# Optimization experiments

Hardware: AMD Instinct MI355X
Metric: run time of the kernel (lower is better)

Reference implementation:

```python
import jax, jax.numpy as jnp
import numpy as np

B, S, D_IN, H, SD = 512, 1024, 64, 64, 4


def setup_inputs() -> dict:
    key = jax.random.key(0)
    ks = jax.random.split(key, 12)
    sc_in = 1.0 / np.sqrt(D_IN)
    sc_h = 1.0 / np.sqrt(H)
    sc_c = 1.0 / np.sqrt(SD + H)
    return {
        "x": jax.random.normal(ks[0], (B, S, D_IN), jnp.float32),
        "W1": jax.random.uniform(ks[1], (H, D_IN), jnp.float32, -sc_in, sc_in),
        "b1": jax.random.uniform(ks[2], (H,), jnp.float32, -sc_in, sc_in),
        "ln_g": jnp.ones((H,), jnp.float32),
        "ln_b": jnp.zeros((H,), jnp.float32),
        "Wi": jax.random.uniform(ks[3], (SD, H), jnp.float32, -sc_h, sc_h),
        "bi": jax.random.uniform(ks[4], (SD,), jnp.float32, -sc_h, sc_h),
        "Wc1": jax.random.uniform(ks[5], (H, SD + H), jnp.float32, -sc_c, sc_c),
        "bc1": jax.random.uniform(ks[6], (H,), jnp.float32, -sc_c, sc_c),
        "Wc2": jax.random.uniform(ks[7], (SD, H), jnp.float32, -sc_h, sc_h),
        "bc2": jax.random.uniform(ks[8], (SD,), jnp.float32, -sc_h, sc_h),
        "corr_scale": jnp.asarray(0.01, jnp.float32),
        "A_level": jnp.zeros((1,), jnp.float32),
        "A_trend": jnp.zeros((1,), jnp.float32),
        "A_gamma": jnp.zeros((1,), jnp.float32),
        "A_resid": jnp.zeros((1,), jnp.float32),
        "omega": jnp.zeros((1,), jnp.float32),
    }


def reference(x, W1, b1, ln_g, ln_b, Wi, bi, Wc1, bc1, Wc2, bc2,
              corr_scale, A_level, A_trend, A_gamma, A_resid, omega):
    # input_proj: Linear -> LayerNorm -> GELU (exact erf), dropout=0
    h = jnp.einsum('bsd,hd->bsh', x, W1) + b1
    mu = jnp.mean(h, axis=-1, keepdims=True)
    var = jnp.mean((h - mu) ** 2, axis=-1, keepdims=True)
    h = (h - mu) * jax.lax.rsqrt(var + 1e-5) * ln_g + ln_b
    h = jax.nn.gelu(h, approximate=False)  # [B,S,H]

    # structured A for state_dim == 4: diag(a_l, a_t, gamma*cos(w), a_r)
    a_l = jax.nn.sigmoid(A_level) * 0.15 + 0.85
    a_t = jax.nn.sigmoid(A_trend) * 0.25 + 0.7
    gamma = jax.nn.sigmoid(A_gamma) * 0.2 + 0.8
    a_r = jax.nn.sigmoid(A_resid) * 0.4
    A = jnp.diag(jnp.concatenate([a_l, a_t, gamma * jnp.cos(omega), a_r]))  # [4,4]

    # innovation applied to all steps at once (batched tiny GEMM)
    bx = jnp.einsum('bsh,kh->bsk', h, Wi) + bi  # [B,S,4]

    def step(s, inp):
        bx_t, h_t = inp  # [B,4], [B,H]
        s_lin = s @ A.T + bx_t
        corr_in = jnp.concatenate([s_lin, h_t], axis=-1)  # [B,4+H]
        c = jax.nn.gelu(corr_in @ Wc1.T + bc1, approximate=False) @ Wc2.T + bc2
        s_new = s_lin + corr_scale * jnp.tanh(c)
        return s_new, s_new

    s0 = jnp.zeros((x.shape[0], SD), x.dtype)
    _, outs = jax.lax.scan(step, s0, (bx.transpose(1, 0, 2), h.transpose(1, 0, 2)))
    return outs.transpose(1, 0, 2)  # [B,S,4] == return_all_states=True
```

## Files before the change

### kernel.cpp

```cpp
#include <hip/hip_runtime.h>
#include <hip/hip_bf16.h>

#define BB 512
#define SS 1024
#define DIN 64
#define HH 64
#define SD4 4
#define CH 64
#define LB 64

typedef __attribute__((ext_vector_type(8))) short s8v;
typedef __attribute__((ext_vector_type(4))) float f4v;

#define MFMA_BF16(a, b, c) __builtin_amdgcn_mfma_f32_16x16x32_bf16((a), (b), (c), 0, 0, 0)

template <int CTRL>
__device__ __forceinline__ float dppf(float v) {
    return __int_as_float(__builtin_amdgcn_mov_dpp(__float_as_int(v), CTRL, 0xF, 0xF, false));
}

__device__ __forceinline__ float rcp_fast(float x) {
    return __builtin_amdgcn_rcpf(x);
}
__device__ __forceinline__ unsigned int cvt_pk(float lo, float hi) {
    unsigned int r;
    asm("v_cvt_pk_bf16_f32 %0, %1, %2" : "=v"(r) : "v"(lo), "v"(hi));
    return r;
}
__device__ __forceinline__ float bf2f(unsigned short u) {
    return __uint_as_float(((unsigned int)u) << 16);
}
__device__ __forceinline__ float sigmoid_f(float x) {
    return 1.0f / (1.0f + __expf(-x));
}
__device__ __forceinline__ float tanh_fast(float x) {
    return fmaf(-2.0f, rcp_fast(__expf(2.0f * x) + 1.0f), 1.0f);
}
__device__ __forceinline__ float gelu_fast(float x) {
    float x2 = x * x;
    float z = x * fmaf(x2, -0.0713548162f, -1.5957691216f);
    return x * rcp_fast(1.0f + __expf(z));
}
__device__ __forceinline__ s8v cvt8(const float* __restrict__ p) {
    const float4* q4 = (const float4*)p;
    float4 a = q4[0], b = q4[1];
    union { s8v s; unsigned int u[4]; } r;
    r.u[0] = cvt_pk(a.x, a.y); r.u[1] = cvt_pk(a.z, a.w);
    r.u[2] = cvt_pk(b.x, b.y); r.u[3] = cvt_pk(b.z, b.w);
    return r.s;
}

__global__ __launch_bounds__(256)
void prep_mfma(const float* __restrict__ x,
               const float* __restrict__ W1, const float* __restrict__ b1,
               const float* __restrict__ ln_g, const float* __restrict__ ln_b,
               const float* __restrict__ Wi, const float* __restrict__ bi,
               const float* __restrict__ Wc1, const float* __restrict__ bc1,
               uint2* __restrict__ pre4, float* __restrict__ bx)
{
    __shared__ unsigned short hb[4][16 * 88];
    __shared__ unsigned short wcs[64 * 72];

    const int tid = threadIdx.x;
    const int wave = tid >> 6;
    const int lane = tid & 63;
    const int c = lane & 15;
    const int q = lane >> 4;

    const long tokW = ((long)blockIdx.x * 4 + wave) * 64;

    const float* xp = x + (tokW + c) * DIN + q * 8;
    float4 xf0 = *(const float4*)(xp + 0);
    float4 xf1 = *(const float4*)(xp + 4);
    float4 xf2 = *(const float4*)(xp + 32);
    float4 xf3 = *(const float4*)(xp + 36);
    xp += 16 * DIN;

    {
        const int row = tid >> 2, chn = tid & 3;
        const float4* s4 = (const float4*)(Wc1 + row * 68 + 4 + chn * 16);
        float4 f0 = s4[0], f1 = s4[1], f2 = s4[2], f3 = s4[3];
        uint2* dst = (uint2*)(wcs + row * 72 + chn * 16);
        dst[0] = make_uint2(cvt_pk(f0.x, f0.y), cvt_pk(f0.z, f0.w));
        dst[1] = make_uint2(cvt_pk(f1.x, f1.y), cvt_pk(f1.z, f1.w));
        dst[2] = make_uint2(cvt_pk(f2.x, f2.y), cvt_pk(f2.z, f2.w));
        dst[3] = make_uint2(cvt_pk(f3.x, f3.y), cvt_pk(f3.z, f3.w));
    }
    __syncthreads();

    s8v W1f[4][2], Wif[2];
#pragma unroll
    for (int n = 0; n < 4; ++n)
#pragma unroll
        for (int kh = 0; kh < 2; ++kh)
            W1f[n][kh] = cvt8(W1 + (4 * c + n) * DIN + q * 8 + kh * 32);
#pragma unroll
    for (int kh = 0; kh < 2; ++kh) {
        if (c < 4) {
            Wif[kh] = cvt8(Wi + c * HH + q * 8 + kh * 32);
        } else {
            s8v z;
#pragma unroll
            for (int e = 0; e < 8; ++e) z[e] = 0;
            Wif[kh] = z;
        }
    }

    float gln[4], bln[4], b1v[4], bc1v[4];
#pragma unroll
    for (int n = 0; n < 4; ++n) {
        const int j1 = 4 * c + n;
        const int j2 = c + 16 * n;
        gln[n] = ln_g[j1]; bln[n] = ln_b[j1]; b1v[n] = b1[j1];
        bc1v[n] = bc1[j2];
    }
    const float biv = (c < 4) ? bi[c] : 0.0f;

    unsigned short* Hb = hb[wave];
    uint2* pq = pre4 + (tokW + q * 4) * 16 + c;
    float* bq = bx + (tokW + q * 4) * SD4 + c;

    auto gemm1_ln = [&](s8v A0_, s8v A1_, uint2* hwo) {
        f4v acc[4];
#pragma unroll
        for (int n = 0; n < 4; ++n) {
            f4v z = { b1v[n], b1v[n], b1v[n], b1v[n] };
            z = MFMA_BF16(A0_, W1f[n][0], z);
            acc[n] = MFMA_BF16(A1_, W1f[n][1], z);
        }
        float sm[4], sq[4];
#pragma unroll
        for (int r = 0; r < 4; ++r) {
            sm[r] = acc[0][r] + acc[1][r] + acc[2][r] + acc[3][r];
            sq[r] = fmaf(acc[0][r], acc[0][r],
                    fmaf(acc[1][r], acc[1][r],
                    fmaf(acc[2][r], acc[2][r], acc[3][r] * acc[3][r])));
        }
#pragma unroll
        for (int r = 0; r < 4; ++r) { sm[r] += dppf<0x121>(sm[r]); sq[r] += dppf<0x121>(sq[r]); }
#pragma unroll
        for (int r = 0; r < 4; ++r) { sm[r] += dppf<0x122>(sm[r]); sq[r] += dppf<0x122>(sq[r]); }
#pragma unroll
        for (int r = 0; r < 4; ++r) { sm[r] += dppf<0x124>(sm[r]); sq[r] += dppf<0x124>(sq[r]); }
#pragma unroll
        for (int r = 0; r < 4; ++r) { sm[r] += dppf<0x128>(sm[r]); sq[r] += dppf<0x128>(sq[r]); }
#pragma unroll
        for (int r = 0; r < 4; ++r) {
            const float mu = sm[r] * (1.0f / HH);
            const float var = fmaf(-mu, mu, sq[r] * (1.0f / HH));
            const float rstd = rsqrtf(var + 1e-5f);
            float g0 = gelu_fast(fmaf((acc[0][r] - mu) * rstd, gln[0], bln[0]));
            float g1 = gelu_fast(fmaf((acc[1][r] - mu) * rstd, gln[1], bln[1]));
            float g2 = gelu_fast(fmaf((acc[2][r] - mu) * rstd, gln[2], bln[2]));
            float g3 = gelu_fast(fmaf((acc[3][r] - mu) * rstd, gln[3], bln[3]));
            hwo[r] = make_uint2(cvt_pk(g0, g1), cvt_pk(g2, g3));
        }
    };

    s8v A0, A1;
    {
        union { s8v s; unsigned int u[4]; } a;
        a.u[0] = cvt_pk(xf0.x, xf0.y); a.u[1] = cvt_pk(xf0.z, xf0.w);
        a.u[2] = cvt_pk(xf1.x, xf1.y); a.u[3] = cvt_pk(xf1.z, xf1.w);
        A0 = a.s;
        a.u[0] = cvt_pk(xf2.x, xf2.y); a.u[1] = cvt_pk(xf2.z, xf2.w);
        a.u[2] = cvt_pk(xf3.x, xf3.y); a.u[3] = cvt_pk(xf3.z, xf3.w);
        A1 = a.s;
    }
    xf0 = *(const float4*)(xp + 0);
    xf1 = *(const float4*)(xp + 4);
    xf2 = *(const float4*)(xp + 32);
    xf3 = *(const float4*)(xp + 36);
    xp += 16 * DIN;

    uint2 hw[4];
    gemm1_ln(A0, A1, hw);
#pragma unroll
    for (int r = 0; r < 4; ++r) *(uint2*)(Hb + (q * 4 + r) * 88 + 4 * c) = hw[r];

#pragma unroll 1
    for (int t = 0; t < 4; ++t) {
        s8v H0 = *(const s8v*)(Hb + c * 88 + q * 8);
        s8v H1 = *(const s8v*)(Hb + c * 88 + 32 + q * 8);

        uint2 hwn[4];
        if (t < 3) {
            union { s8v s; unsigned int u[4]; } a;
            a.u[0] = cvt_pk(xf0.x, xf0.y); a.u[1] = cvt_pk(xf0.z, xf0.w);
            a.u[2] = cvt_pk(xf1.x, xf1.y); a.u[3] = cvt_pk(xf1.z, xf1.w);
            s8v nA0 = a.s;
            a.u[0] = cvt_pk(xf2.x, xf2.y); a.u[1] = cvt_pk(xf2.z, xf2.w);
            a.u[2] = cvt_pk(xf3.x, xf3.y); a.u[3] = cvt_pk(xf3.z, xf3.w);
            s8v nA1 = a.s;
            if (t < 2) {
                xf0 = *(const float4*)(xp + 0);
                xf1 = *(const float4*)(xp + 4);
                xf2 = *(const float4*)(xp + 32);
                xf3 = *(const float4*)(xp + 36);
                xp += 16 * DIN;
            }
            gemm1_ln(nA0, nA1, hwn);
        }

        f4v p[4];
#pragma unroll
        for (int n = 0; n < 4; ++n) {
            const s8v Wf0 = *(const s8v*)(wcs + (c + 16 * n) * 72 + q * 8);
            const s8v Wf1 = *(const s8v*)(wcs + (c + 16 * n) * 72 + 32 + q * 8);
            f4v z = { bc1v[n], bc1v[n], bc1v[n], bc1v[n] };
            z = MFMA_BF16(H0, Wf0, z);
            p[n] = MFMA_BF16(H1, Wf1, z);
        }
        f4v bz = { biv, biv, biv, biv };
        bz = MFMA_BF16(H0, Wif[0], bz);
        bz = MFMA_BF16(H1, Wif[1], bz);

        if (c < 4) {
#pragma unroll
            for (int r = 0; r < 4; ++r) bq[r * SD4] = bz[r];
        }
#pragma unroll
        for (int r = 0; r < 4; ++r)
            pq[r * 16] = make_uint2(cvt_pk(p[0][r], p[1][r]),
                                    cvt_pk(p[2][r], p[3][r]));
        pq += 256; bq += 64;

        if (t < 3) {
#pragma unroll
            for (int r = 0; r < 4; ++r) *(uint2*)(Hb + (q * 4 + r) * 88 + 4 * c) = hwn[r];
        }
    }
}

__global__ __launch_bounds__(256)
void scan_chunk(const uint2* __restrict__ pre4, const float* __restrict__ bx,
                const float* __restrict__ Wc1, const float* __restrict__ Wc2,
                const float* __restrict__ bc2, const float* __restrict__ corr_scale,
                const float* __restrict__ A_level, const float* __restrict__ A_trend,
                const float* __restrict__ A_gamma, const float* __restrict__ A_resid,
                const float* __restrict__ omega, float* __restrict__ out)
{
    const int tid = threadIdx.x;
    const int task = blockIdx.x * 16 + (tid >> 4);
    const int L = tid & 15;
    const int ci = task >> 9;
    const int b = task & 511;
    const int warm = (ci * CH < LB) ? ci * CH : LB;
    const int t0 = ci * CH - warm;
    const int nsteps = warm + CH;

    float w[4][4], v[4][4];
#pragma unroll
    for (int m = 0; m < 4; ++m) {
        const int j = L + 16 * m;
#pragma unroll
        for (int k = 0; k < 4; ++k) {
            w[m][k] = Wc1[j * 68 + k];
            v[k][m] = Wc2[k * HH + j];
        }
    }
    const float cs = corr_scale[0];
    const float a0 = sigmoid_f(A_level[0]) * 0.15f + 0.85f;
    const float a1 = sigmoid_f(A_trend[0]) * 0.25f + 0.70f;
    const float a2 = (sigmoid_f(A_gamma[0]) * 0.2f + 0.8f) * cosf(omega[0]);
    const float a3 = sigmoid_f(A_resid[0]) * 0.4f;
    const float csel = bc2[L & 3];
    const bool o1 = (L & 1) != 0;
    const bool o2 = (L & 2) != 0;

    const uint2* pp = pre4 + ((long)b * SS + t0) * 16 + L;
    const float4* bp = (const float4*)bx + (long)b * SS + t0;
    float* op = out + ((long)b * SS + t0) * SD4;

    float s0 = 0.f, s1 = 0.f, s2 = 0.f, s3 = 0.f;

    uint2 pv[4]; float4 bv[4];
#pragma unroll
    for (int i = 0; i < 4; ++i) { pv[i] = pp[(long)i * 16]; bv[i] = bp[i]; }

#pragma unroll 2
    for (int tt = 0; tt < nsteps; tt += 4) {
        const int ntt = (tt + 4 < nsteps) ? (tt + 4) : (nsteps - 4);
        const uint2* qp = pp + (long)ntt * 16;
        const float4* qb = bp + ntt;
        uint2 np[4]; float4 nb[4];
#pragma unroll
        for (int i = 0; i < 4; ++i) { np[i] = qp[i * 16]; nb[i] = qb[i]; }

        const bool wr = (tt >= warm);
#pragma unroll
        for (int i = 0; i < 4; ++i) {
            const float l0 = fmaf(a0, s0, bv[i].x);
            const float l1 = fmaf(a1, s1, bv[i].y);
            const float l2 = fmaf(a2, s2, bv[i].z);
            const float l3 = fmaf(a3, s3, bv[i].w);
            const float p0 = bf2f((unsigned short)(pv[i].x & 0xffffu));
            const float p1 = bf2f((unsigned short)(pv[i].x >> 16));
            const float p2 = bf2f((unsigned short)(pv[i].y & 0xffffu));
            const float p3 = bf2f((unsigned short)(pv[i].y >> 16));
            float g[4];
            {
                float ua0 = fmaf(l0, w[0][0], p0), ub0 = fmaf(l2, w[0][2], l3 * w[0][3]);
                float ua1 = fmaf(l0, w[1][0], p1), ub1 = fmaf(l2, w[1][2], l3 * w[1][3]);
                float ua2 = fmaf(l0, w[2][0], p2), ub2 = fmaf(l2, w[2][2], l3 * w[2][3]);
                float ua3 = fmaf(l0, w[3][0], p3), ub3 = fmaf(l2, w[3][2], l3 * w[3][3]);
                g[0] = gelu_fast(fmaf(l1, w[0][1], ua0) + ub0);
                g[1] = gelu_fast(fmaf(l1, w[1][1], ua1) + ub1);
                g[2] = gelu_fast(fmaf(l1, w[2][1], ua2) + ub2);
                g[3] = gelu_fast(fmaf(l1, w[3][1], ua3) + ub3);
            }
            const float P0 = fmaf(g[0], v[0][0], g[1] * v[0][1]) + fmaf(g[2], v[0][2], g[3] * v[0][3]);
            const float P1 = fmaf(g[0], v[1][0], g[1] * v[1][1]) + fmaf(g[2], v[1][2], g[3] * v[1][3]);
            const float P2 = fmaf(g[0], v[2][0], g[1] * v[2][1]) + fmaf(g[2], v[2][2], g[3] * v[2][3]);
            const float P3 = fmaf(g[0], v[3][0], g[1] * v[3][1]) + fmaf(g[2], v[3][2], g[3] * v[3][3]);
            const float k0 = o1 ? P1 : P0, s0s = o1 ? P0 : P1;
            const float k1 = o1 ? P3 : P2, s1s = o1 ? P2 : P3;
            const float Af = k0 + dppf<0xB1>(s0s);
            const float Bf = k1 + dppf<0xB1>(s1s);
            const float kk = o2 ? Bf : Af, ss = o2 ? Af : Bf;
            float T = kk + dppf<0x4E>(ss);
            T += dppf<0x124>(T);
            T += dppf<0x128>(T);
            const float th = tanh_fast(T + csel);
            const float lsel = o2 ? (o1 ? l3 : l2) : (o1 ? l1 : l0);
            const float sval = fmaf(cs, th, lsel);
            s0 = dppf<0x00>(sval);
            s1 = dppf<0x55>(sval);
            s2 = dppf<0xAA>(sval);
            s3 = dppf<0xFF>(sval);
            if (wr && L < 4) op[(tt + i) * SD4 + L] = sval;
        }
#pragma unroll
        for (int i = 0; i < 4; ++i) { pv[i] = np[i]; bv[i] = nb[i]; }
    }
}

extern "C" void kernel_launch(void* const* d_in, const int* in_sizes, int n_in,
                              void* d_out, int out_size, void* d_ws, size_t ws_size,
                              hipStream_t stream) {
    (void)in_sizes; (void)n_in; (void)out_size; (void)ws_size;
    const float* x    = (const float*)d_in[0];
    const float* W1   = (const float*)d_in[1];
    const float* b1   = (const float*)d_in[2];
    const float* ln_g = (const float*)d_in[3];
    const float* ln_b = (const float*)d_in[4];
    const float* Wi   = (const float*)d_in[5];
    const float* bi   = (const float*)d_in[6];
    const float* Wc1  = (const float*)d_in[7];
    const float* bc1  = (const float*)d_in[8];
    const float* Wc2  = (const float*)d_in[9];
    const float* bc2  = (const float*)d_in[10];
    const float* corr = (const float*)d_in[11];
    const float* Al   = (const float*)d_in[12];
    const float* At   = (const float*)d_in[13];
    const float* Ag   = (const float*)d_in[14];
    const float* Ar   = (const float*)d_in[15];
    const float* om   = (const float*)d_in[16];

    uint2* pre4 = (uint2*)d_ws;
    float* bx = (float*)((char*)d_ws + (size_t)BB * SS * 16 * sizeof(uint2));
    float* out = (float*)d_out;

    prep_mfma<<<dim3(2048), dim3(256), 0, stream>>>(
        x, W1, b1, ln_g, ln_b, Wi, bi, Wc1, bc1, pre4, bx);
    scan_chunk<<<dim3(BB * SS / CH / 16), dim3(256), 0, stream>>>(
        pre4, bx, Wc1, Wc2, bc2, corr, Al, At, Ag, Ar, om, out);
}
```

Measured before the change: 298.2 us.

## Reorder pre-activation layout for 16-byte loads and map one batch row per block

The prep kernel now writes the bf16 pre-activations in a token-quad-major layout with two 16-byte stores per lane instead of four 8-byte stores. The scan reads each 4-step group with wide uint4 loads and launches one block per batch row, with each 16-lane group handling one chunk. Each group runs a fixed 128-step loop (64 warm-up plus 64 output steps). Outputs are gathered into one register per lane and written as a single coalesced store per 4 steps. The trade-offs are fewer blocks, redundant steps for chunk 0 (now 128 instead of 64), and a two-deep prefetch with unroll 1.

```diff
diff --git a/kernel.cpp b/kernel.cpp
--- a/kernel.cpp
+++ b/kernel.cpp
@@ -117,7 +117,7 @@
     const float biv = (c < 4) ? bi[c] : 0.0f;
 
     unsigned short* Hb = hb[wave];
-    uint2* pq = pre4 + (tokW + q * 4) * 16 + c;
+    uint2* pq = pre4 + ((tokW >> 2) + q) * 64 + c * 4;
     float* bq = bx + (tokW + q * 4) * SD4 + c;
 
     auto gemm1_ln = [&](s8v A0_, s8v A1_, uint2* hwo) {
@@ -219,10 +219,14 @@
 #pragma unroll
             for (int r = 0; r < 4; ++r) bq[r * SD4] = bz[r];
         }
-#pragma unroll
-        for (int r = 0; r < 4; ++r)
-            pq[r * 16] = make_uint2(cvt_pk(p[0][r], p[1][r]),
-                                    cvt_pk(p[2][r], p[3][r]));
+        {
+            uint2 u0 = make_uint2(cvt_pk(p[0][0], p[1][0]), cvt_pk(p[2][0], p[3][0]));
+            uint2 u1 = make_uint2(cvt_pk(p[0][1], p[1][1]), cvt_pk(p[2][1], p[3][1]));
+            uint2 u2 = make_uint2(cvt_pk(p[0][2], p[1][2]), cvt_pk(p[2][2], p[3][2]));
+            uint2 u3 = make_uint2(cvt_pk(p[0][3], p[1][3]), cvt_pk(p[2][3], p[3][3]));
+            *(uint4*)(pq)     = make_uint4(u0.x, u0.y, u1.x, u1.y);
+            *(uint4*)(pq + 2) = make_uint4(u2.x, u2.y, u3.x, u3.y);
+        }
         pq += 256; bq += 64;
 
         if (t < 3) {
@@ -241,13 +245,13 @@
                 const float* __restrict__ omega, float* __restrict__ out)
 {
     const int tid = threadIdx.x;
-    const int task = blockIdx.x * 16 + (tid >> 4);
+    const int g = tid >> 4;
     const int L = tid & 15;
-    const int ci = task >> 9;
-    const int b = task & 511;
-    const int warm = (ci * CH < LB) ? ci * CH : LB;
-    const int t0 = ci * CH - warm;
-    const int nsteps = warm + CH;
+    const int b = blockIdx.x;
+    const int warm = (g == 0) ? 0 : LB;
+    const int t0 = g * CH - warm;
+    const int wend = warm + CH;
+    const int myi = L >> 2;
 
     float w[4][4], v[4][4];
 #pragma unroll
@@ -268,51 +272,41 @@
     const bool o1 = (L & 1) != 0;
     const bool o2 = (L & 2) != 0;
 
-    const uint2* pp = pre4 + ((long)b * SS + t0) * 16 + L;
+    const uint4* pp = (const uint4*)pre4 + (((long)b * SS + t0) >> 2) * 32 + L * 2;
     const float4* bp = (const float4*)bx + (long)b * SS + t0;
     float* op = out + ((long)b * SS + t0) * SD4;
 
     float s0 = 0.f, s1 = 0.f, s2 = 0.f, s3 = 0.f;
 
-    uint2 pv[4]; float4 bv[4];
-#pragma unroll
-    for (int i = 0; i < 4; ++i) { pv[i] = pp[(long)i * 16]; bv[i] = bp[i]; }
-
-#pragma unroll 2
-    for (int tt = 0; tt < nsteps; tt += 4) {
-        const int ntt = (tt + 4 < nsteps) ? (tt + 4) : (nsteps - 4);
-        const uint2* qp = pp + (long)ntt * 16;
-        const float4* qb = bp + ntt;
-        uint2 np[4]; float4 nb[4];
-#pragma unroll
-        for (int i = 0; i < 4; ++i) { np[i] = qp[i * 16]; nb[i] = qb[i]; }
-
-        const bool wr = (tt >= warm);
+    auto step4 = [&](uint4 qa, uint4 qb, const float4* bv, int tt) {
+        float oreg = 0.f;
 #pragma unroll
         for (int i = 0; i < 4; ++i) {
+            const unsigned int ux = (i == 0) ? qa.x : (i == 1) ? qa.z : (i == 2) ? qb.x : qb.z;
+            const unsigned int uy = (i == 0) ? qa.y : (i == 1) ? qa.w : (i == 2) ? qb.y : qb.w;
             const float l0 = fmaf(a0, s0, bv[i].x);
             const float l1 = fmaf(a1, s1, bv[i].y);
             const float l2 = fmaf(a2, s2, bv[i].z);
             const float l3 = fmaf(a3, s3, bv[i].w);
-            const float p0 = bf2f((unsigned short)(pv[i].x & 0xffffu));
-            const float p1 = bf2f((unsigned short)(pv[i].x >> 16));
-            const float p2 = bf2f((unsigned short)(pv[i].y & 0xffffu));
-            const float p3 = bf2f((unsigned short)(pv[i].y >> 16));
-            float g[4];
+            const float p0 = bf2f((unsigned short)(ux & 0xffffu));
+            const float p1 = bf2f((unsigned short)(ux >> 16));
+            const float p2 = bf2f((unsigned short)(uy & 0xffffu));
+            const float p3 = bf2f((unsigned short)(uy >> 16));
+            float gg[4];
             {
                 float ua0 = fmaf(l0, w[0][0], p0), ub0 = fmaf(l2, w[0][2], l3 * w[0][3]);
                 float ua1 = fmaf(l0, w[1][0], p1), ub1 = fmaf(l2, w[1][2], l3 * w[1][3]);
                 float ua2 = fmaf(l0, w[2][0], p2), ub2 = fmaf(l2, w[2][2], l3 * w[2][3]);
                 float ua3 = fmaf(l0, w[3][0], p3), ub3 = fmaf(l2, w[3][2], l3 * w[3][3]);
-                g[0] = gelu_fast(fmaf(l1, w[0][1], ua0) + ub0);
-                g[1] = gelu_fast(fmaf(l1, w[1][1], ua1) + ub1);
-                g[2] = gelu_fast(fmaf(l1, w[2][1], ua2) + ub2);
-                g[3] = gelu_fast(fmaf(l1, w[3][1], ua3) + ub3);
+                gg[0] = gelu_fast(fmaf(l1, w[0][1], ua0) + ub0);
+                gg[1] = gelu_fast(fmaf(l1, w[1][1], ua1) + ub1);
+                gg[2] = gelu_fast(fmaf(l1, w[2][1], ua2) + ub2);
+                gg[3] = gelu_fast(fmaf(l1, w[3][1], ua3) + ub3);
             }
-            const float P0 = fmaf(g[0], v[0][0], g[1] * v[0][1]) + fmaf(g[2], v[0][2], g[3] * v[0][3]);
-            const float P1 = fmaf(g[0], v[1][0], g[1] * v[1][1]) + fmaf(g[2], v[1][2], g[3] * v[1][3]);
-            const float P2 = fmaf(g[0], v[2][0], g[1] * v[2][1]) + fmaf(g[2], v[2][2], g[3] * v[2][3]);
-            const float P3 = fmaf(g[0], v[3][0], g[1] * v[3][1]) + fmaf(g[2], v[3][2], g[3] * v[3][3]);
+            const float P0 = fmaf(gg[0], v[0][0], gg[1] * v[0][1]) + fmaf(gg[2], v[0][2], gg[3] * v[0][3]);
+            const float P1 = fmaf(gg[0], v[1][0], gg[1] * v[1][1]) + fmaf(gg[2], v[1][2], gg[3] * v[1][3]);
+            const float P2 = fmaf(gg[0], v[2][0], gg[1] * v[2][1]) + fmaf(gg[2], v[2][2], gg[3] * v[2][3]);
+            const float P3 = fmaf(gg[0], v[3][0], gg[1] * v[3][1]) + fmaf(gg[2], v[3][2], gg[3] * v[3][3]);
             const float k0 = o1 ? P1 : P0, s0s = o1 ? P0 : P1;
             const float k1 = o1 ? P3 : P2, s1s = o1 ? P2 : P3;
             const float Af = k0 + dppf<0xB1>(s0s);
@@ -328,10 +322,35 @@
             s1 = dppf<0x55>(sval);
             s2 = dppf<0xAA>(sval);
             s3 = dppf<0xFF>(sval);
-            if (wr && L < 4) op[(tt + i) * SD4 + L] = sval;
-        }
-#pragma unroll
-        for (int i = 0; i < 4; ++i) { pv[i] = np[i]; bv[i] = nb[i]; }
+            if (myi == i) oreg = sval;
+        }
+        if (tt >= warm && tt < wend) op[tt * SD4 + L] = oreg;
+    };
+
+    uint4 qa0 = pp[0],  qb0 = pp[1];
+    uint4 qa1 = pp[32], qb1 = pp[33];
+    float4 bA[4], bB[4];
+#pragma unroll
+    for (int i = 0; i < 4; ++i) { bA[i] = bp[i]; bB[i] = bp[4 + i]; }
+
+#pragma unroll 1
+    for (int tt = 0; tt < 2 * CH; tt += 8) {
+        const int pf0 = (tt + 8  < 2 * CH) ? (tt + 8)  : (2 * CH - 8);
+        const int pf1 = (tt + 12 < 2 * CH) ? (tt + 12) : (2 * CH - 8);
+        const uint4* p0 = pp + (pf0 >> 2) * 32;
+        const uint4* p1 = pp + (pf1 >> 2) * 32;
+        uint4 nqa0 = p0[0], nqb0 = p0[1];
+        uint4 nqa1 = p1[0], nqb1 = p1[1];
+        float4 nbA[4], nbB[4];
+#pragma unroll
+        for (int i = 0; i < 4; ++i) { nbA[i] = bp[pf0 + i]; nbB[i] = bp[pf1 + i]; }
+
+        step4(qa0, qb0, bA, tt);
+        step4(qa1, qb1, bB, tt + 4);
+
+        qa0 = nqa0; qb0 = nqb0; qa1 = nqa1; qb1 = nqb1;
+#pragma unroll
+        for (int i = 0; i < 4; ++i) { bA[i] = nbA[i]; bB[i] = nbB[i]; }
     }
 }
 
@@ -363,6 +382,6 @@
 
     prep_mfma<<<dim3(2048), dim3(256), 0, stream>>>(
         x, W1, b1, ln_g, ln_b, Wi, bi, Wc1, bc1, pre4, bx);
-    scan_chunk<<<dim3(BB * SS / CH / 16), dim3(256), 0, stream>>>(
+    scan_chunk<<<dim3(BB), dim3(256), 0, stream>>>(
         pre4, bx, Wc1, Wc2, bc2, corr, Al, At, Ag, Ar, om, out);
 }
```

Measured after the change: 299.5 us. No clear change (+0.4%).
